# Optimization experiments

Hardware: AMD Instinct MI355X
Metric: run time of the kernel (lower is better)

## Reference

```python
import jax, jax.numpy as jnp
import numpy as np

EMBED_DIM = 2048
NUM_HEADS = 16
HEAD_DIM = EMBED_DIM // NUM_HEADS  # 128
GROUP = 256
NEG = -1e9


def setup_inputs() -> dict:
    key = jax.random.key(0)
    ks = jax.random.split(key, 4)
    B, N, C = 2, 8192, EMBED_DIM
    s = 1.0 / np.sqrt(C).astype(np.float32)
    return {
        "x": jax.random.normal(ks[0], (B, N, C), jnp.float32),
        "Wq": jax.random.normal(ks[1], (C, C), jnp.float32) * s,
        "bq": jnp.zeros((C,), jnp.float32),
        "Wk": jax.random.normal(ks[2], (C, C), jnp.float32) * s,
        "bk": jnp.zeros((C,), jnp.float32),
        "Wv": jax.random.normal(ks[3], (C, C), jnp.float32) * s,
        "bv": jnp.zeros((C,), jnp.float32),
    }


def _s2_attn(x, Wq, bq, Wk, bk, Wv, bv):
    B, N, C = x.shape
    H, hd, gs = NUM_HEADS, HEAD_DIM, GROUP
    G = N // gs
    half = H // 2

    def heads(t):  # [B,N,C] -> [B,H,N,hd]
        return t.reshape(B, N, H, hd).transpose(0, 2, 1, 3)

    q = heads(x @ Wq.T + bq)
    k = heads(x @ Wk.T + bk)
    v = heads(x @ Wv.T + bv)

    def shift(t, s):  # shift second half of heads along sequence
        return jnp.concatenate([t[:, :half], jnp.roll(t[:, half:], s, axis=2)], axis=1)

    q, k, v = shift(q, -(gs // 2)), shift(k, -(gs // 2)), shift(v, -(gs // 2))

    # group-local attention: [B,H,G,gs,hd]
    qg = q.reshape(B, H, G, gs, hd)
    kg = k.reshape(B, H, G, gs, hd)
    vg = v.reshape(B, H, G, gs, hd)

    scores = jnp.einsum("bhgqd,bhgkd->bhgqk", qg, kg) / np.sqrt(hd).astype(x.dtype)
    causal = jnp.triu(jnp.ones((gs, gs), bool), 1)  # mask strictly-upper triangle
    scores = jnp.where(causal, NEG, scores)
    attn = jax.nn.softmax(scores, axis=-1)
    out = jnp.einsum("bhgqk,bhgkd->bhgqd", attn, vg).reshape(B, H, N, hd)

    out = shift(out, gs // 2)  # un-shift the shifted heads
    return out.transpose(0, 2, 1, 3).reshape(B, N, C)


def reference(x, Wq, bq, Wk, bk, Wv, bv):
    return _s2_attn(x, Wq, bq, Wk, bk, Wv, bv)
```

## Files before the change

### kernel.cpp

```cpp
#include <hip/hip_runtime.h>
#include <hip/hip_bf16.h>

#define NSEQ 8192
#define CDIM 2048
#define NHEAD 16
#define HD 128

typedef short short8 __attribute__((ext_vector_type(8)));
typedef short short4v __attribute__((ext_vector_type(4)));
typedef float float4v __attribute__((ext_vector_type(4)));

__device__ __forceinline__ short f2bf(float f) {
    __hip_bfloat16 h = __float2bfloat16(f);
    return *reinterpret_cast<short*>(&h);
}

__device__ __forceinline__ void async_load16(const short* g, short* l) {
    __builtin_amdgcn_global_load_lds((const __attribute__((address_space(1))) void*)g,
                                     (__attribute__((address_space(3))) void*)l,
                                     16, 0, 0);
}

#define X8 (33554432 / 8)
#define W8 (4194304 / 8)

__global__ __launch_bounds__(256) void cvt_all(
    const float* __restrict__ x, const float* __restrict__ wq,
    const float* __restrict__ wk, const float* __restrict__ wv,
    short* __restrict__ xb, short* __restrict__ wqb,
    short* __restrict__ wkb, short* __restrict__ wvb)
{
    const size_t i = (size_t)blockIdx.x * blockDim.x + threadIdx.x;
    const float* src;
    short* dst;
    size_t off;
    if (i < X8)              { src = x;  dst = xb;  off = i; }
    else if (i < X8 + W8)    { src = wq; dst = wqb; off = i - X8; }
    else if (i < X8 + 2*W8)  { src = wk; dst = wkb; off = i - X8 - W8; }
    else                     { src = wv; dst = wvb; off = i - X8 - 2*(size_t)W8; }
    const float4v a = ((const float4v*)src)[off * 2];
    const float4v b = ((const float4v*)src)[off * 2 + 1];
    short8 o;
    for (int j = 0; j < 4; j++) { o[j] = f2bf(a[j]); o[4 + j] = f2bf(b[j]); }
    ((short8*)dst)[off] = o;
}

#define PBAR()  asm volatile("s_barrier" ::: "memory")
#define LGKM0() do { asm volatile("s_waitcnt lgkmcnt(0)" ::: "memory"); \
                     __builtin_amdgcn_sched_barrier(0); } while (0)
#define VMC4()  asm volatile("s_waitcnt vmcnt(4)" ::: "memory")
#define VMC0()  asm volatile("s_waitcnt vmcnt(0)" ::: "memory")

#define MFMA(d, x, y) d = __builtin_amdgcn_mfma_f32_16x16x32_bf16(x, y, d, 0, 0, 0)

__global__ __launch_bounds__(512, 2) void qkv_gemm8(
    const short* __restrict__ xb,
    const short* __restrict__ Wq, const float* __restrict__ bq,
    const short* __restrict__ Wk, const float* __restrict__ bk,
    const short* __restrict__ Wv, const float* __restrict__ bv,
    float* __restrict__ qout, short* __restrict__ kt, short* __restrict__ vt)
{
    __shared__ short lds[2][2][256 * 64];

    const int tid  = threadIdx.x;
    const int w    = tid >> 6;
    const int lane = tid & 63;
    const int quad = lane >> 4;
    const int l15  = lane & 15;
    const int wm   = w >> 2;
    const int wn   = w & 3;

    const int id    = (blockIdx.x & 7) * 192 + (blockIdx.x >> 3);
    const int mtile = id / 24;
    const int rest  = id - mtile * 24;
    const int mat   = rest >> 3;
    const int ntile = rest & 7;
    const int M0 = mtile << 8;
    const int N0 = ntile << 8;

    const short* W    = (mat == 0) ? Wq : (mat == 1) ? Wk : Wv;
    const float* bias = (mat == 0) ? bq : (mat == 1) ? bk : bv;
    const short* Ab = xb + (size_t)M0 * CDIM;
    const short* Bb = W  + (size_t)N0 * CDIM;

    const int stg_row = tid >> 3;
    const int stg_col = ((tid & 7) * 8) ^ (((tid >> 3) & 7) << 3);
    const int cswz    = (lane & 7) << 3;

    float bvals[4];
#pragma unroll
    for (int j = 0; j < 4; ++j)
        bvals[j] = bias[N0 + wn * 64 + j * 16 + l15];
    VMC0();

    float4v acc[8][4];
#pragma unroll
    for (int i = 0; i < 8; ++i)
#pragma unroll
        for (int j = 0; j < 4; ++j)
            acc[i][j] = (float4v){0.f, 0.f, 0.f, 0.f};

    auto stage = [&](int bufi, int ab, int h, int t, const short* src) {
        short* l0 = &lds[bufi][ab][h * 8192 + w * 512];
        const short* g = src + (size_t)(h * 128 + stg_row) * CDIM + t * 64 + stg_col;
        async_load16(g, l0);
        async_load16(g + (size_t)64 * CDIM, l0 + 4096);
    };
    auto ldA = [&](int bufi, int i, int ks) -> short8 {
        const int row = wm * 128 + i * 16 + l15;
        return *(const short8*)&lds[bufi][0][row * 64 + ((ks * 32 + quad * 8) ^ cswz)];
    };
    auto ldB = [&](int bufi, int j, int ks) -> short8 {
        const int row = wn * 64 + j * 16 + l15;
        return *(const short8*)&lds[bufi][1][row * 64 + ((ks * 32 + quad * 8) ^ cswz)];
    };

    stage(0, 0, 0, 0, Ab); stage(0, 0, 1, 0, Ab);
    stage(0, 1, 0, 0, Bb); stage(0, 1, 1, 0, Bb);
    stage(1, 1, 0, 1, Bb); stage(1, 1, 1, 1, Bb);
    VMC4();
    PBAR();

    short8 a[4][2], b[4][2];
    for (int it = 0; it < 16; ++it) {
        const int t1 = 2 * it + 1;
        const int t2 = (2 * it + 2 > 31) ? 31 : 2 * it + 2;
        const int t3 = (2 * it + 3 > 31) ? 31 : 2 * it + 3;

#pragma unroll
        for (int i = 0; i < 4; ++i) { a[i][0] = ldA(0, i, 0); a[i][1] = ldA(0, i, 1); }
#pragma unroll
        for (int j = 0; j < 2; ++j) { b[j][0] = ldB(0, j, 0); b[j][1] = ldB(0, j, 1); }
        stage(1, 0, 0, t1, Ab); stage(1, 0, 1, t1, Ab);
        PBAR(); LGKM0();
        __builtin_amdgcn_s_setprio(1);
#pragma unroll
        for (int i = 0; i < 4; ++i)
#pragma unroll
            for (int j = 0; j < 2; ++j) { MFMA(acc[i][j], a[i][0], b[j][0]);
                                          MFMA(acc[i][j], a[i][1], b[j][1]); }
        __builtin_amdgcn_s_setprio(0);
        PBAR();

#pragma unroll
        for (int j = 2; j < 4; ++j) { b[j][0] = ldB(0, j, 0); b[j][1] = ldB(0, j, 1); }
        PBAR(); LGKM0();
        __builtin_amdgcn_s_setprio(1);
#pragma unroll
        for (int i = 0; i < 4; ++i)
#pragma unroll
            for (int j = 2; j < 4; ++j) { MFMA(acc[i][j], a[i][0], b[j][0]);
                                          MFMA(acc[i][j], a[i][1], b[j][1]); }
        __builtin_amdgcn_s_setprio(0);
        PBAR();

#pragma unroll
        for (int i = 0; i < 4; ++i) { a[i][0] = ldA(0, 4 + i, 0); a[i][1] = ldA(0, 4 + i, 1); }
        stage(0, 1, 0, t2, Bb);
        PBAR(); LGKM0();
        __builtin_amdgcn_s_setprio(1);
#pragma unroll
        for (int i = 0; i < 4; ++i)
#pragma unroll
            for (int j = 2; j < 4; ++j) { MFMA(acc[4 + i][j], a[i][0], b[j][0]);
                                          MFMA(acc[4 + i][j], a[i][1], b[j][1]); }
        __builtin_amdgcn_s_setprio(0);
        PBAR();

        stage(0, 1, 1, t2, Bb);
        PBAR(); LGKM0();
        __builtin_amdgcn_s_setprio(1);
#pragma unroll
        for (int i = 0; i < 4; ++i)
#pragma unroll
            for (int j = 0; j < 2; ++j) { MFMA(acc[4 + i][j], a[i][0], b[j][0]);
                                          MFMA(acc[4 + i][j], a[i][1], b[j][1]); }
        __builtin_amdgcn_s_setprio(0);
        VMC4();
        PBAR();

#pragma unroll
        for (int i = 0; i < 4; ++i) { a[i][0] = ldA(1, i, 0); a[i][1] = ldA(1, i, 1); }
#pragma unroll
        for (int j = 0; j < 2; ++j) { b[j][0] = ldB(1, j, 0); b[j][1] = ldB(1, j, 1); }
        stage(0, 0, 0, t2, Ab); stage(0, 0, 1, t2, Ab);
        PBAR(); LGKM0();
        __builtin_amdgcn_s_setprio(1);
#pragma unroll
        for (int i = 0; i < 4; ++i)
#pragma unroll
            for (int j = 0; j < 2; ++j) { MFMA(acc[i][j], a[i][0], b[j][0]);
                                          MFMA(acc[i][j], a[i][1], b[j][1]); }
        __builtin_amdgcn_s_setprio(0);
        PBAR();

#pragma unroll
        for (int j = 2; j < 4; ++j) { b[j][0] = ldB(1, j, 0); b[j][1] = ldB(1, j, 1); }
        PBAR(); LGKM0();
        __builtin_amdgcn_s_setprio(1);
#pragma unroll
        for (int i = 0; i < 4; ++i)
#pragma unroll
            for (int j = 2; j < 4; ++j) { MFMA(acc[i][j], a[i][0], b[j][0]);
                                          MFMA(acc[i][j], a[i][1], b[j][1]); }
        __builtin_amdgcn_s_setprio(0);
        PBAR();

#pragma unroll
        for (int i = 0; i < 4; ++i) { a[i][0] = ldA(1, 4 + i, 0); a[i][1] = ldA(1, 4 + i, 1); }
        stage(1, 1, 0, t3, Bb);
        PBAR(); LGKM0();
        __builtin_amdgcn_s_setprio(1);
#pragma unroll
        for (int i = 0; i < 4; ++i)
#pragma unroll
            for (int j = 2; j < 4; ++j) { MFMA(acc[4 + i][j], a[i][0], b[j][0]);
                                          MFMA(acc[4 + i][j], a[i][1], b[j][1]); }
        __builtin_amdgcn_s_setprio(0);
        PBAR();

        stage(1, 1, 1, t3, Bb);
        PBAR(); LGKM0();
        __builtin_amdgcn_s_setprio(1);
#pragma unroll
        for (int i = 0; i < 4; ++i)
#pragma unroll
            for (int j = 0; j < 2; ++j) { MFMA(acc[4 + i][j], a[i][0], b[j][0]);
                                          MFMA(acc[4 + i][j], a[i][1], b[j][1]); }
        __builtin_amdgcn_s_setprio(0);
        VMC4();
        PBAR();
    }

#pragma unroll
    for (int j = 0; j < 4; ++j) {
        const int n = N0 + wn * 64 + j * 16 + l15;
        if (mat == 0) {
#pragma unroll
            for (int i = 0; i < 8; ++i) {
                const int mrow = M0 + wm * 128 + i * 16 + quad * 4;
#pragma unroll
                for (int r = 0; r < 4; ++r)
                    qout[((size_t)(mrow + r) << 11) + n] = acc[i][j][r] + bvals[j];
            }
        } else if (mat == 1) {
            const int h = n >> 7;
            const int d = n & (HD - 1);
#pragma unroll
            for (int i = 0; i < 8; ++i) {
                const int mrow = M0 + wm * 128 + i * 16 + quad * 4;
#pragma unroll
                for (int r = 0; r < 4; ++r) {
                    const int m  = mrow + r;
                    const int bb = m >> 13;
                    const int sq = m & (NSEQ - 1);
                    kt[(((size_t)(bb * NHEAD + h) * NSEQ + sq) << 7) + d] =
                        f2bf(acc[i][j][r] + bvals[j]);
                }
            }
        } else {
            const int h = n >> 7;
            const int d = n & (HD - 1);
#pragma unroll
            for (int i = 0; i < 8; ++i) {
                const int mrow = M0 + wm * 128 + i * 16 + quad * 4;
                const int bb = mrow >> 13;
                const int sq = mrow & (NSEQ - 1);
                short4v o4;
#pragma unroll
                for (int r = 0; r < 4; ++r) o4[r] = f2bf(acc[i][j][r] + bvals[j]);
                *(short4v*)&vt[(((size_t)(bb * NHEAD + h) * HD + d) << 13) + sq] = o4;
            }
        }
    }
}

__global__ __launch_bounds__(512, 1) void s2_attn(const float* qsrc,
                                                  const short* __restrict__ kt,
                                                  const short* __restrict__ vt,
                                                  float* out)
{
    __shared__ short Ks[64 * 136];
    __shared__ short Vt[2][128 * 64];
    __shared__ short Ps[8][32 * 40];

    const int bx = blockIdx.x;
    const int g  = bx & 31;
    const int h  = (bx >> 5) & 15;
    const int b  = bx >> 9;
    const int shift = (h >= 8) ? 128 : 0;
    const int sbase = g * 256 + shift;

    const int tid  = threadIdx.x;
    const int wave = tid >> 6;
    const int lane = tid & 63;
    const int quad = lane >> 4;
    const int l15  = lane & 15;

    const size_t bh = ((size_t)b * NHEAD + h) * NSEQ;
    const short* kg = kt + bh * HD;
    const short* vg = vt + bh * HD;

    const int mt0 = wave * 2;

    const int vrow_in_w = lane >> 3;
    const int vgcol     = ((lane & 7) * 8) ^ (vrow_in_w << 3);
    const int krow0 = tid >> 4;
    const int kcolb = (tid & 15) * 8;

    short8 kr0, kr1;

    {
        const int p = (sbase + vgcol) & (NSEQ - 1);
#pragma unroll
        for (int c = 0; c < 2; c++) {
            const int d = c * 64 + wave * 8 + vrow_in_w;
            async_load16(vg + (size_t)d * NSEQ + p, &Vt[0][(c * 64 + wave * 8) * 64]);
        }
        const int p0 = (sbase + krow0) & (NSEQ - 1);
        const int p1 = (sbase + krow0 + 32) & (NSEQ - 1);
        kr0 = *(const short8*)(kg + (size_t)p0 * HD + kcolb);
        kr1 = *(const short8*)(kg + (size_t)p1 * HD + kcolb);
    }

    short8 qf[2][4];
#pragma unroll
    for (int im = 0; im < 2; im++) {
        const int row = (mt0 + im) * 16 + l15;
        const int p   = (sbase + row) & (NSEQ - 1);
        const float* qr = qsrc + (((size_t)(b * NSEQ + p)) << 11) + h * HD;
#pragma unroll
        for (int ks = 0; ks < 4; ks++) {
            const float4v qa = *(const float4v*)(qr + ks * 32 + quad * 8);
            const float4v qb = *(const float4v*)(qr + ks * 32 + quad * 8 + 4);
            short8 f;
#pragma unroll
            for (int j = 0; j < 4; j++) { f[j] = f2bf(qa[j]); f[4 + j] = f2bf(qb[j]); }
            qf[im][ks] = f;
        }
    }

    const float4v fzero = {0.f, 0.f, 0.f, 0.f};
    float4v o[2][8];
#pragma unroll
    for (int im = 0; im < 2; im++)
#pragma unroll
        for (int dt = 0; dt < 8; dt++)
            o[im][dt] = fzero;
    float rs[2][4] = {{0.f, 0.f, 0.f, 0.f}, {0.f, 0.f, 0.f, 0.f}};

    for (int kc = 0; kc < 4; kc++) {
        VMC0();
        *(short8*)&Ks[krow0 * 136 + kcolb]        = kr0;
        *(short8*)&Ks[(krow0 + 32) * 136 + kcolb] = kr1;
        LGKM0();
        PBAR();

        if (kc < 3) {
            const int p = (sbase + (kc + 1) * 64 + vgcol) & (NSEQ - 1);
#pragma unroll
            for (int c = 0; c < 2; c++) {
                const int d = c * 64 + wave * 8 + vrow_in_w;
                async_load16(vg + (size_t)d * NSEQ + p,
                             &Vt[(kc + 1) & 1][(c * 64 + wave * 8) * 64]);
            }
            const int p0 = (sbase + (kc + 1) * 64 + krow0) & (NSEQ - 1);
            const int p1 = (sbase + (kc + 1) * 64 + krow0 + 32) & (NSEQ - 1);
            kr0 = *(const short8*)(kg + (size_t)p0 * HD + kcolb);
            kr1 = *(const short8*)(kg + (size_t)p1 * HD + kcolb);
        }

        float4v s[2][4];
#pragma unroll
        for (int im = 0; im < 2; im++)
#pragma unroll
            for (int nn = 0; nn < 4; nn++)
                s[im][nn] = fzero;
        __builtin_amdgcn_s_setprio(1);
#pragma unroll
        for (int nn = 0; nn < 4; nn++) {
            short8 kf[4];
#pragma unroll
            for (int ks = 0; ks < 4; ks++)
                kf[ks] = *(const short8*)&Ks[(nn * 16 + l15) * 136 + ks * 32 + quad * 8];
#pragma unroll
            for (int im = 0; im < 2; im++)
#pragma unroll
                for (int ks = 0; ks < 4; ks++)
                    s[im][nn] = __builtin_amdgcn_mfma_f32_16x16x32_bf16(
                        qf[im][ks], kf[ks], s[im][nn], 0, 0, 0);
        }
        __builtin_amdgcn_s_setprio(0);

#pragma unroll
        for (int half = 0; half < 2; half++) {
#pragma unroll
            for (int im = 0; im < 2; im++) {
                const int qpos = (mt0 + im) * 16 + quad * 4;
#pragma unroll
                for (int nn2 = 0; nn2 < 2; nn2++) {
                    const int nn   = half * 2 + nn2;
                    const int kpos = kc * 64 + nn * 16 + l15;
#pragma unroll
                    for (int r = 0; r < 4; r++) {
                        const float sv = s[im][nn][r] * 0.088388347648318447f;
                        const float pv = (kpos > qpos + r)
                                             ? 0.f
                                             : __expf(fminf(sv, 30.f));
                        rs[im][r] += pv;
                        Ps[wave][(im * 16 + quad * 4 + r) * 40 + nn2 * 16 + l15] = f2bf(pv);
                    }
                }
            }
            LGKM0();
            short8 pf[2];
#pragma unroll
            for (int im = 0; im < 2; im++)
                pf[im] = *(const short8*)&Ps[wave][(im * 16 + l15) * 40 + quad * 8];
            __builtin_amdgcn_s_setprio(1);
#pragma unroll
            for (int dt = 0; dt < 8; dt++) {
                const int d = dt * 16 + l15;
                const short8 vf = *(const short8*)
                    &Vt[kc & 1][d * 64 + ((half * 32 + quad * 8) ^ ((l15 & 7) << 3))];
#pragma unroll
                for (int im = 0; im < 2; im++)
                    o[im][dt] = __builtin_amdgcn_mfma_f32_16x16x32_bf16(
                        pf[im], vf, o[im][dt], 0, 0, 0);
            }
            __builtin_amdgcn_s_setprio(0);
        }
        PBAR();
    }

#pragma unroll
    for (int im = 0; im < 2; im++)
#pragma unroll
        for (int r = 0; r < 4; r++) {
            float v = rs[im][r];
            v += __shfl_xor(v, 1);
            v += __shfl_xor(v, 2);
            v += __shfl_xor(v, 4);
            v += __shfl_xor(v, 8);
            rs[im][r] = v;
        }

#pragma unroll
    for (int im = 0; im < 2; im++) {
#pragma unroll
        for (int r = 0; r < 4; r++) {
            const int row = (mt0 + im) * 16 + quad * 4 + r;
            const int p   = (sbase + row) & (NSEQ - 1);
            const float inv = 1.f / rs[im][r];
            const size_t obase = (((size_t)(b * NSEQ + p)) << 11) + h * HD;
#pragma unroll
            for (int dt = 0; dt < 8; dt++)
                out[obase + dt * 16 + l15] = o[im][dt][r] * inv;
        }
    }
}

extern "C" void kernel_launch(void* const* d_in, const int* in_sizes, int n_in,
                              void* d_out, int out_size, void* d_ws, size_t ws_size,
                              hipStream_t stream) {
    (void)in_sizes; (void)n_in; (void)out_size; (void)ws_size;
    const float* x  = (const float*)d_in[0];
    const float* Wq = (const float*)d_in[1];
    const float* bq = (const float*)d_in[2];
    const float* Wk = (const float*)d_in[3];
    const float* bk = (const float*)d_in[4];
    const float* Wv = (const float*)d_in[5];
    const float* bv = (const float*)d_in[6];

    short* xb  = (short*)d_ws;
    short* wqb = xb  + (size_t)33554432;
    short* wkb = wqb + (size_t)4194304;
    short* wvb = wkb + (size_t)4194304;
    short* kt  = wvb + (size_t)4194304;
    short* vt  = kt  + (size_t)33554432;

    float* outp = (float*)d_out;

    cvt_all<<<dim3(22528), 256, 0, stream>>>(x, Wq, Wk, Wv, xb, wqb, wkb, wvb);
    qkv_gemm8<<<dim3(1536), 512, 0, stream>>>(xb, wqb, bq, wkb, bk, wvb, bv,
                                              outp, kt, vt);
    s2_attn<<<dim3(1024), 512, 0, stream>>>(outp, kt, vt, outp);
}
```

Baseline: 736.6 us.

## Skip fully masked causal tiles in attention and split QKV GEMM per matrix

The attention kernel reassigns each wave's two query tiles to rows wave and wave+8, which balances causal work across waves. It then skips QK^T MFMAs, softmax writes and PV MFMAs for key half-chunks lying entirely above the diagonal. Separately, the fused QKV GEMM launch is split into three launches, one per weight matrix, with a simpler tile mapping. The skipping removes roughly half the attention matrix math. The extra kernel launches and the loss of cross-matrix reuse of the x tile in L2 could cost some time in the GEMM.

```diff
diff --git a/kernel.cpp b/kernel.cpp
--- a/kernel.cpp
+++ b/kernel.cpp
@@ -55,10 +55,9 @@
 
 __global__ __launch_bounds__(512, 2) void qkv_gemm8(
     const short* __restrict__ xb,
-    const short* __restrict__ Wq, const float* __restrict__ bq,
-    const short* __restrict__ Wk, const float* __restrict__ bk,
-    const short* __restrict__ Wv, const float* __restrict__ bv,
-    float* __restrict__ qout, short* __restrict__ kt, short* __restrict__ vt)
+    const short* __restrict__ W, const float* __restrict__ bias,
+    float* __restrict__ qout, short* __restrict__ kt, short* __restrict__ vt,
+    const int mat)
 {
     __shared__ short lds[2][2][256 * 64];
 
@@ -70,16 +69,12 @@
     const int wm   = w >> 2;
     const int wn   = w & 3;
 
-    const int id    = (blockIdx.x & 7) * 192 + (blockIdx.x >> 3);
-    const int mtile = id / 24;
-    const int rest  = id - mtile * 24;
-    const int mat   = rest >> 3;
-    const int ntile = rest & 7;
+    const int id    = (blockIdx.x & 7) * 64 + (blockIdx.x >> 3);
+    const int mtile = id >> 3;
+    const int ntile = id & 7;
     const int M0 = mtile << 8;
     const int N0 = ntile << 8;
 
-    const short* W    = (mat == 0) ? Wq : (mat == 1) ? Wk : Wv;
-    const float* bias = (mat == 0) ? bq : (mat == 1) ? bk : bv;
     const short* Ab = xb + (size_t)M0 * CDIM;
     const short* Bb = W  + (size_t)N0 * CDIM;
 
@@ -301,7 +296,8 @@
     const short* kg = kt + bh * HD;
     const short* vg = vt + bh * HD;
 
-    const int mt0 = wave * 2;
+    const int mtA = wave;
+    const int mtB = wave + 8;
 
     const int vrow_in_w = lane >> 3;
     const int vgcol     = ((lane & 7) * 8) ^ (vrow_in_w << 3);
@@ -326,7 +322,8 @@
     short8 qf[2][4];
 #pragma unroll
     for (int im = 0; im < 2; im++) {
-        const int row = (mt0 + im) * 16 + l15;
+        const int mt  = im ? mtB : mtA;
+        const int row = mt * 16 + l15;
         const int p   = (sbase + row) & (NSEQ - 1);
         const float* qr = qsrc + (((size_t)(b * NSEQ + p)) << 11) + h * HD;
 #pragma unroll
@@ -370,6 +367,9 @@
             kr1 = *(const short8*)(kg + (size_t)p1 * HD + kcolb);
         }
 
+        const bool hA[2] = {(4 * kc)     <= mtA, (4 * kc + 2) <= mtA};
+        const bool hB[2] = {(4 * kc)     <= mtB, (4 * kc + 2) <= mtB};
+
         float4v s[2][4];
 #pragma unroll
         for (int im = 0; im < 2; im++)
@@ -379,24 +379,34 @@
         __builtin_amdgcn_s_setprio(1);
 #pragma unroll
         for (int nn = 0; nn < 4; nn++) {
-            short8 kf[4];
-#pragma unroll
-            for (int ks = 0; ks < 4; ks++)
-                kf[ks] = *(const short8*)&Ks[(nn * 16 + l15) * 136 + ks * 32 + quad * 8];
-#pragma unroll
-            for (int im = 0; im < 2; im++)
+            const int hh = nn >> 1;
+            if (hB[hh]) {
+                short8 kf[4];
 #pragma unroll
                 for (int ks = 0; ks < 4; ks++)
-                    s[im][nn] = __builtin_amdgcn_mfma_f32_16x16x32_bf16(
-                        qf[im][ks], kf[ks], s[im][nn], 0, 0, 0);
+                    kf[ks] = *(const short8*)&Ks[(nn * 16 + l15) * 136 + ks * 32 + quad * 8];
+                if (hA[hh]) {
+#pragma unroll
+                    for (int ks = 0; ks < 4; ks++)
+                        s[0][nn] = __builtin_amdgcn_mfma_f32_16x16x32_bf16(
+                            qf[0][ks], kf[ks], s[0][nn], 0, 0, 0);
+                }
+#pragma unroll
+                for (int ks = 0; ks < 4; ks++)
+                    s[1][nn] = __builtin_amdgcn_mfma_f32_16x16x32_bf16(
+                        qf[1][ks], kf[ks], s[1][nn], 0, 0, 0);
+            }
         }
         __builtin_amdgcn_s_setprio(0);
 
 #pragma unroll
         for (int half = 0; half < 2; half++) {
+            if (!hB[half]) continue;
 #pragma unroll
             for (int im = 0; im < 2; im++) {
-                const int qpos = (mt0 + im) * 16 + quad * 4;
+                if (im == 0 && !hA[half]) continue;
+                const int mt   = im ? mtB : mtA;
+                const int qpos = mt * 16 + quad * 4;
 #pragma unroll
                 for (int nn2 = 0; nn2 < 2; nn2++) {
                     const int nn   = half * 2 + nn2;
@@ -414,19 +424,20 @@
             }
             LGKM0();
             short8 pf[2];
-#pragma unroll
-            for (int im = 0; im < 2; im++)
-                pf[im] = *(const short8*)&Ps[wave][(im * 16 + l15) * 40 + quad * 8];
+            if (hA[half])
+                pf[0] = *(const short8*)&Ps[wave][(0 * 16 + l15) * 40 + quad * 8];
+            pf[1] = *(const short8*)&Ps[wave][(1 * 16 + l15) * 40 + quad * 8];
             __builtin_amdgcn_s_setprio(1);
 #pragma unroll
             for (int dt = 0; dt < 8; dt++) {
                 const int d = dt * 16 + l15;
                 const short8 vf = *(const short8*)
                     &Vt[kc & 1][d * 64 + ((half * 32 + quad * 8) ^ ((l15 & 7) << 3))];
-#pragma unroll
-                for (int im = 0; im < 2; im++)
-                    o[im][dt] = __builtin_amdgcn_mfma_f32_16x16x32_bf16(
-                        pf[im], vf, o[im][dt], 0, 0, 0);
+                if (hA[half])
+                    o[0][dt] = __builtin_amdgcn_mfma_f32_16x16x32_bf16(
+                        pf[0], vf, o[0][dt], 0, 0, 0);
+                o[1][dt] = __builtin_amdgcn_mfma_f32_16x16x32_bf16(
+                    pf[1], vf, o[1][dt], 0, 0, 0);
             }
             __builtin_amdgcn_s_setprio(0);
         }
@@ -447,9 +458,10 @@
 
 #pragma unroll
     for (int im = 0; im < 2; im++) {
+        const int mt = im ? mtB : mtA;
 #pragma unroll
         for (int r = 0; r < 4; r++) {
-            const int row = (mt0 + im) * 16 + quad * 4 + r;
+            const int row = mt * 16 + quad * 4 + r;
             const int p   = (sbase + row) & (NSEQ - 1);
             const float inv = 1.f / rs[im][r];
             const size_t obase = (((size_t)(b * NSEQ + p)) << 11) + h * HD;
@@ -482,7 +494,8 @@
     float* outp = (float*)d_out;
 
     cvt_all<<<dim3(22528), 256, 0, stream>>>(x, Wq, Wk, Wv, xb, wqb, wkb, wvb);
-    qkv_gemm8<<<dim3(1536), 512, 0, stream>>>(xb, wqb, bq, wkb, bk, wvb, bv,
-                                              outp, kt, vt);
+    qkv_gemm8<<<dim3(512), 512, 0, stream>>>(xb, wqb, bq, outp, kt, vt, 0);
+    qkv_gemm8<<<dim3(512), 512, 0, stream>>>(xb, wkb, bk, outp, kt, vt, 1);
+    qkv_gemm8<<<dim3(512), 512, 0, stream>>>(xb, wvb, bv, outp, kt, vt, 2);
     s2_attn<<<dim3(1024), 512, 0, stream>>>(outp, kt, vt, outp);
 }
```

Result: no change. 746.6 us (+1.4%).
